# Kernel tuning notes

Measured on AMD Instinct MI355X. Metric: run time of the kernel, lower is better.

Reference implementation:

```python
import jax, jax.numpy as jnp
import numpy as np

B, T, D = 64, 4096, 256


def setup_inputs() -> dict:
    key = jax.random.key(0)
    k0, k1, k2, k3 = jax.random.split(key, 4)
    q = jax.random.normal(k0, (B, D), dtype=jnp.float32)
    k = jax.random.normal(k1, (B, T, D), dtype=jnp.float32)
    m = jax.random.uniform(k2, (B, T), dtype=jnp.float32)
    # learned params: torch.rand init for weights, zeros for bias
    W = jax.random.uniform(k3, (D, D), dtype=jnp.float32)
    bias = jnp.zeros((1,), dtype=jnp.float32)
    return {"q": q, "k": k, "m": m, "W": W, "bias": bias}


def reference(q, k, m, W, bias):
    # mids = W @ q   (original repeats W over batch; a single einsum suffices)
    mids = jnp.einsum('de,be->bd', W, q)            # [B, D]
    # scores_bt = tanh(k_bt . mids_b + bias)
    scores = jnp.tanh(jnp.einsum('btd,bd->bt', k, mids) + bias)  # [B, T]
    # masked, max-stabilized softmax over time
    scores = scores - jnp.max(scores, axis=1, keepdims=True)
    e = jnp.exp(scores) * m
    attn = e / jnp.sum(e, axis=1, keepdims=True)
    return attn
```

## Files before the change

kernel.cpp:

```cpp
#include <hip/hip_runtime.h>
#include <math.h>


#define BB 64
#define TT 4096
#define DD 256
#define TBLKS 32
#define RPB (TT / TBLKS)
#define GB 8
#define CHUNK (TT / GB)

__device__ __forceinline__ float fast_tanh(float x) {
    float e = __expf(2.0f * x);
    return 1.0f - 2.0f * __builtin_amdgcn_rcpf(1.0f + e);
}

__global__ __launch_bounds__(256) void mids_kernel(const float* __restrict__ q,
                                                   const float* __restrict__ W,
                                                   float* __restrict__ mids) {
    const int b    = blockIdx.x;
    const int seg  = blockIdx.y;
    const int lane = threadIdx.x & 63;
    const int wave = threadIdx.x >> 6;
    const int grp  = lane >> 4;
    const int l16  = lane & 15;

    const float* qb = q + (size_t)b * DD + l16 * 4;
    const float4 qf0 = *(const float4*)(qb + 0);
    const float4 qf1 = *(const float4*)(qb + 64);
    const float4 qf2 = *(const float4*)(qb + 128);
    const float4 qf3 = *(const float4*)(qb + 192);

    const int d0 = seg * 64 + wave * 16;
    #pragma unroll
    for (int g = 0; g < 4; ++g) {
        const int d = d0 + g * 4 + grp;
        const float* wr = W + (size_t)d * DD + l16 * 4;
        const float4 w0 = *(const float4*)(wr + 0);
        const float4 w1 = *(const float4*)(wr + 64);
        const float4 w2 = *(const float4*)(wr + 128);
        const float4 w3 = *(const float4*)(wr + 192);
        float p = w0.x*qf0.x + w0.y*qf0.y + w0.z*qf0.z + w0.w*qf0.w;
        p += w1.x*qf1.x + w1.y*qf1.y + w1.z*qf1.z + w1.w*qf1.w;
        p += w2.x*qf2.x + w2.y*qf2.y + w2.z*qf2.z + w2.w*qf2.w;
        p += w3.x*qf3.x + w3.y*qf3.y + w3.z*qf3.z + w3.w*qf3.w;
        p += __shfl_xor(p, 1, 64);
        p += __shfl_xor(p, 2, 64);
        p += __shfl_xor(p, 4, 64);
        p += __shfl_xor(p, 8, 64);
        if (l16 == 0) mids[b * DD + d] = p;
    }
}

__global__ __launch_bounds__(256) void scores_kernel(const float* __restrict__ k,
                                                     const float* __restrict__ mids,
                                                     const float* __restrict__ bias,
                                                     float* __restrict__ scores,
                                                     float* __restrict__ partmax) {
    const int b    = blockIdx.x;
    const int tb   = blockIdx.y;
    const int lane = threadIdx.x & 63;
    const int wave = threadIdx.x >> 6;
    const int grp  = lane >> 4;
    const int l16  = lane & 15;
    const float bv = bias[0];

    const float* mb = mids + (size_t)b * DD + l16 * 4;
    const float4 mf0 = *(const float4*)(mb + 0);
    const float4 mf1 = *(const float4*)(mb + 64);
    const float4 mf2 = *(const float4*)(mb + 128);
    const float4 mf3 = *(const float4*)(mb + 192);

    const int t0 = tb * RPB + wave * 32;
    const float* kbase = k + ((size_t)b * TT + t0) * DD + l16 * 4;

    float lmax = -2.0f;
    #pragma unroll 2
    for (int g = 0; g < 8; ++g) {
        const int trow = g * 4 + grp;
        const float* kr = kbase + (size_t)trow * DD;
        const float4 k0 = *(const float4*)(kr + 0);
        const float4 k1 = *(const float4*)(kr + 64);
        const float4 k2 = *(const float4*)(kr + 128);
        const float4 k3 = *(const float4*)(kr + 192);
        float p = k0.x*mf0.x + k0.y*mf0.y + k0.z*mf0.z + k0.w*mf0.w;
        p += k1.x*mf1.x + k1.y*mf1.y + k1.z*mf1.z + k1.w*mf1.w;
        p += k2.x*mf2.x + k2.y*mf2.y + k2.z*mf2.z + k2.w*mf2.w;
        p += k3.x*mf3.x + k3.y*mf3.y + k3.z*mf3.z + k3.w*mf3.w;
        p += __shfl_xor(p, 1, 64);
        p += __shfl_xor(p, 2, 64);
        p += __shfl_xor(p, 4, 64);
        p += __shfl_xor(p, 8, 64);
        const float s = fast_tanh(p + bv);
        lmax = fmaxf(lmax, s);
        if (l16 == 0) scores[b * TT + t0 + trow] = s;
    }
    lmax = fmaxf(lmax, __shfl_xor(lmax, 16, 64));
    lmax = fmaxf(lmax, __shfl_xor(lmax, 32, 64));
    __shared__ float wmax[4];
    if (lane == 0) wmax[wave] = lmax;
    __syncthreads();
    if (threadIdx.x == 0)
        partmax[b * TBLKS + tb] =
            fmaxf(fmaxf(wmax[0], wmax[1]), fmaxf(wmax[2], wmax[3]));
}

__global__ __launch_bounds__(256) void exp_kernel(const float* __restrict__ scores,
                                                  const float* __restrict__ m,
                                                  const float* __restrict__ partmax,
                                                  float* __restrict__ out,
                                                  float* __restrict__ blocksum) {
    const int b    = blockIdx.x;
    const int g    = blockIdx.y;
    const int tid  = threadIdx.x;
    const int lane = tid & 63;
    const int wave = tid >> 6;
    __shared__ float smax;
    __shared__ float wsum[4];

    if (wave == 0) {
        float mv = (lane < TBLKS) ? partmax[b * TBLKS + lane] : -2.0f;
        #pragma unroll
        for (int off = 16; off; off >>= 1) mv = fmaxf(mv, __shfl_xor(mv, off, 64));
        if (lane == 0) smax = mv;
    }
    __syncthreads();
    const float maxv = smax;

    const int idx = b * TT + g * CHUNK + tid * 2;
    const float2 sv = *(const float2*)(scores + idx);
    const float2 mv2 = *(const float2*)(m + idx);
    const float e0 = __expf(sv.x - maxv) * mv2.x;
    const float e1 = __expf(sv.y - maxv) * mv2.y;
    *(float2*)(out + idx) = make_float2(e0, e1);

    float local = e0 + e1;
    #pragma unroll
    for (int off = 32; off; off >>= 1) local += __shfl_xor(local, off, 64);
    if (lane == 0) wsum[wave] = local;
    __syncthreads();
    if (tid == 0)
        blocksum[b * GB + g] = wsum[0] + wsum[1] + wsum[2] + wsum[3];
}

__global__ __launch_bounds__(256) void norm_kernel(const float* __restrict__ blocksum,
                                                   float* __restrict__ out) {
    const int b   = blockIdx.x;
    const int g   = blockIdx.y;
    const int tid = threadIdx.x;
    float s = 0.0f;
    #pragma unroll
    for (int i = 0; i < GB; ++i) s += blocksum[b * GB + i];
    const float inv = 1.0f / s;
    const int idx = b * TT + g * CHUNK + tid * 2;
    float2 v = *(const float2*)(out + idx);
    v.x *= inv; v.y *= inv;
    *(float2*)(out + idx) = v;
}

extern "C" void kernel_launch(void* const* d_in, const int* in_sizes, int n_in,
                              void* d_out, int out_size, void* d_ws, size_t ws_size,
                              hipStream_t stream) {
    const float* q    = (const float*)d_in[0];
    const float* k    = (const float*)d_in[1];
    const float* m    = (const float*)d_in[2];
    const float* W    = (const float*)d_in[3];
    const float* bias = (const float*)d_in[4];
    float* out = (float*)d_out;

    float* ws       = (float*)d_ws;
    float* mids     = ws;
    float* scores   = mids + BB * DD;
    float* partmax  = scores + BB * TT;
    float* blocksum = partmax + BB * TBLKS;

    mids_kernel<<<dim3(BB, 4), 256, 0, stream>>>(q, W, mids);
    scores_kernel<<<dim3(BB, TBLKS), 256, 0, stream>>>(k, mids, bias, scores, partmax);
    exp_kernel<<<dim3(BB, GB), 256, 0, stream>>>(scores, m, partmax, out, blocksum);
    norm_kernel<<<dim3(BB, GB), 256, 0, stream>>>(blocksum, out);
}
```

Before: 398.1 us.

## Fuse scores and exp kernels, drop max pass, prefetch k rows, DPP reductions

Merges the score and exp kernels into one pass that computes exp(tanh(.))·mask directly and writes partial sums. The max-subtraction step is dropped because tanh is bounded, which removes a kernel launch and the round trip of the scores buffer. Adds register double-buffering of k rows and swaps the shuffle reductions for DPP row reductions. mids_kernel is also split across more blocks. Skipping the max is numerically safe because the scores lie in [-1,1].

```diff
diff --git a/kernel.cpp b/kernel.cpp
--- a/kernel.cpp
+++ b/kernel.cpp
@@ -9,6 +9,20 @@
 #define RPB (TT / TBLKS)
 #define GB 8
 #define CHUNK (TT / GB)
+
+template<int CTRL>
+__device__ __forceinline__ float dpp_add(float x) {
+    int xi = __builtin_bit_cast(int, x);
+    int yi = __builtin_amdgcn_update_dpp(0, xi, CTRL, 0xF, 0xF, true);
+    return x + __builtin_bit_cast(float, yi);
+}
+__device__ __forceinline__ float row16_sum(float p) {
+    p = dpp_add<0xB1>(p);
+    p = dpp_add<0x4E>(p);
+    p = dpp_add<0x141>(p);
+    p = dpp_add<0x140>(p);
+    return p;
+}
 
 __device__ __forceinline__ float fast_tanh(float x) {
     float e = __expf(2.0f * x);
@@ -31,32 +45,26 @@
     const float4 qf2 = *(const float4*)(qb + 128);
     const float4 qf3 = *(const float4*)(qb + 192);
 
-    const int d0 = seg * 64 + wave * 16;
-    #pragma unroll
-    for (int g = 0; g < 4; ++g) {
-        const int d = d0 + g * 4 + grp;
-        const float* wr = W + (size_t)d * DD + l16 * 4;
-        const float4 w0 = *(const float4*)(wr + 0);
-        const float4 w1 = *(const float4*)(wr + 64);
-        const float4 w2 = *(const float4*)(wr + 128);
-        const float4 w3 = *(const float4*)(wr + 192);
-        float p = w0.x*qf0.x + w0.y*qf0.y + w0.z*qf0.z + w0.w*qf0.w;
-        p += w1.x*qf1.x + w1.y*qf1.y + w1.z*qf1.z + w1.w*qf1.w;
-        p += w2.x*qf2.x + w2.y*qf2.y + w2.z*qf2.z + w2.w*qf2.w;
-        p += w3.x*qf3.x + w3.y*qf3.y + w3.z*qf3.z + w3.w*qf3.w;
-        p += __shfl_xor(p, 1, 64);
-        p += __shfl_xor(p, 2, 64);
-        p += __shfl_xor(p, 4, 64);
-        p += __shfl_xor(p, 8, 64);
-        if (l16 == 0) mids[b * DD + d] = p;
-    }
+    const int d = seg * 16 + wave * 4 + grp;
+    const float* wr = W + (size_t)d * DD + l16 * 4;
+    const float4 w0 = *(const float4*)(wr + 0);
+    const float4 w1 = *(const float4*)(wr + 64);
+    const float4 w2 = *(const float4*)(wr + 128);
+    const float4 w3 = *(const float4*)(wr + 192);
+    float p = w0.x*qf0.x + w0.y*qf0.y + w0.z*qf0.z + w0.w*qf0.w;
+    p += w1.x*qf1.x + w1.y*qf1.y + w1.z*qf1.z + w1.w*qf1.w;
+    p += w2.x*qf2.x + w2.y*qf2.y + w2.z*qf2.z + w2.w*qf2.w;
+    p += w3.x*qf3.x + w3.y*qf3.y + w3.z*qf3.z + w3.w*qf3.w;
+    p = row16_sum(p);
+    if (l16 == 0) mids[b * DD + d] = p;
 }
 
-__global__ __launch_bounds__(256) void scores_kernel(const float* __restrict__ k,
-                                                     const float* __restrict__ mids,
-                                                     const float* __restrict__ bias,
-                                                     float* __restrict__ scores,
-                                                     float* __restrict__ partmax) {
+__global__ __launch_bounds__(256) void fused_kernel(const float* __restrict__ k,
+                                                    const float* __restrict__ mids,
+                                                    const float* __restrict__ m,
+                                                    const float* __restrict__ bias,
+                                                    float* __restrict__ out,
+                                                    float* __restrict__ blocksum) {
     const int b    = blockIdx.x;
     const int tb   = blockIdx.y;
     const int lane = threadIdx.x & 63;
@@ -73,74 +81,48 @@
 
     const int t0 = tb * RPB + wave * 32;
     const float* kbase = k + ((size_t)b * TT + t0) * DD + l16 * 4;
+    const float* mrow  = m + (size_t)b * TT + t0;
+    float* orow        = out + (size_t)b * TT + t0;
 
-    float lmax = -2.0f;
-    #pragma unroll 2
+    float4 c0, c1, c2, c3, n0, n1, n2, n3;
+    {
+        const float* kr = kbase + (size_t)grp * DD;
+        c0 = *(const float4*)(kr + 0);
+        c1 = *(const float4*)(kr + 64);
+        c2 = *(const float4*)(kr + 128);
+        c3 = *(const float4*)(kr + 192);
+    }
+    float esum = 0.0f;
+    #pragma unroll
     for (int g = 0; g < 8; ++g) {
-        const int trow = g * 4 + grp;
-        const float* kr = kbase + (size_t)trow * DD;
-        const float4 k0 = *(const float4*)(kr + 0);
-        const float4 k1 = *(const float4*)(kr + 64);
-        const float4 k2 = *(const float4*)(kr + 128);
-        const float4 k3 = *(const float4*)(kr + 192);
-        float p = k0.x*mf0.x + k0.y*mf0.y + k0.z*mf0.z + k0.w*mf0.w;
-        p += k1.x*mf1.x + k1.y*mf1.y + k1.z*mf1.z + k1.w*mf1.w;
-        p += k2.x*mf2.x + k2.y*mf2.y + k2.z*mf2.z + k2.w*mf2.w;
-        p += k3.x*mf3.x + k3.y*mf3.y + k3.z*mf3.z + k3.w*mf3.w;
-        p += __shfl_xor(p, 1, 64);
-        p += __shfl_xor(p, 2, 64);
-        p += __shfl_xor(p, 4, 64);
-        p += __shfl_xor(p, 8, 64);
+        if (g < 7) {
+            const float* kr = kbase + (size_t)((g + 1) * 4 + grp) * DD;
+            n0 = *(const float4*)(kr + 0);
+            n1 = *(const float4*)(kr + 64);
+            n2 = *(const float4*)(kr + 128);
+            n3 = *(const float4*)(kr + 192);
+        }
+        float p = c0.x*mf0.x + c0.y*mf0.y + c0.z*mf0.z + c0.w*mf0.w;
+        p += c1.x*mf1.x + c1.y*mf1.y + c1.z*mf1.z + c1.w*mf1.w;
+        p += c2.x*mf2.x + c2.y*mf2.y + c2.z*mf2.z + c2.w*mf2.w;
+        p += c3.x*mf3.x + c3.y*mf3.y + c3.z*mf3.z + c3.w*mf3.w;
+        p = row16_sum(p);
         const float s = fast_tanh(p + bv);
-        lmax = fmaxf(lmax, s);
-        if (l16 == 0) scores[b * TT + t0 + trow] = s;
+        if (l16 == 0) {
+            const int trow = g * 4 + grp;
+            const float e = __expf(s) * mrow[trow];
+            orow[trow] = e;
+            esum += e;
+        }
+        c0 = n0; c1 = n1; c2 = n2; c3 = n3;
     }
-    lmax = fmaxf(lmax, __shfl_xor(lmax, 16, 64));
-    lmax = fmaxf(lmax, __shfl_xor(lmax, 32, 64));
-    __shared__ float wmax[4];
-    if (lane == 0) wmax[wave] = lmax;
+    esum += __shfl_xor(esum, 16, 64);
+    esum += __shfl_xor(esum, 32, 64);
+    __shared__ float wsum[4];
+    if (lane == 0) wsum[wave] = esum;
     __syncthreads();
     if (threadIdx.x == 0)
-        partmax[b * TBLKS + tb] =
-            fmaxf(fmaxf(wmax[0], wmax[1]), fmaxf(wmax[2], wmax[3]));
-}
-
-__global__ __launch_bounds__(256) void exp_kernel(const float* __restrict__ scores,
-                                                  const float* __restrict__ m,
-                                                  const float* __restrict__ partmax,
-                                                  float* __restrict__ out,
-                                                  float* __restrict__ blocksum) {
-    const int b    = blockIdx.x;
-    const int g    = blockIdx.y;
-    const int tid  = threadIdx.x;
-    const int lane = tid & 63;
-    const int wave = tid >> 6;
-    __shared__ float smax;
-    __shared__ float wsum[4];
-
-    if (wave == 0) {
-        float mv = (lane < TBLKS) ? partmax[b * TBLKS + lane] : -2.0f;
-        #pragma unroll
-        for (int off = 16; off; off >>= 1) mv = fmaxf(mv, __shfl_xor(mv, off, 64));
-        if (lane == 0) smax = mv;
-    }
-    __syncthreads();
-    const float maxv = smax;
-
-    const int idx = b * TT + g * CHUNK + tid * 2;
-    const float2 sv = *(const float2*)(scores + idx);
-    const float2 mv2 = *(const float2*)(m + idx);
-    const float e0 = __expf(sv.x - maxv) * mv2.x;
-    const float e1 = __expf(sv.y - maxv) * mv2.y;
-    *(float2*)(out + idx) = make_float2(e0, e1);
-
-    float local = e0 + e1;
-    #pragma unroll
-    for (int off = 32; off; off >>= 1) local += __shfl_xor(local, off, 64);
-    if (lane == 0) wsum[wave] = local;
-    __syncthreads();
-    if (tid == 0)
-        blocksum[b * GB + g] = wsum[0] + wsum[1] + wsum[2] + wsum[3];
+        blocksum[b * TBLKS + tb] = (wsum[0] + wsum[1]) + (wsum[2] + wsum[3]);
 }
 
 __global__ __launch_bounds__(256) void norm_kernel(const float* __restrict__ blocksum,
@@ -150,7 +132,7 @@
     const int tid = threadIdx.x;
     float s = 0.0f;
     #pragma unroll
-    for (int i = 0; i < GB; ++i) s += blocksum[b * GB + i];
+    for (int i = 0; i < TBLKS; ++i) s += blocksum[b * TBLKS + i];
     const float inv = 1.0f / s;
     const int idx = b * TT + g * CHUNK + tid * 2;
     float2 v = *(const float2*)(out + idx);
@@ -170,12 +152,9 @@
 
     float* ws       = (float*)d_ws;
     float* mids     = ws;
-    float* scores   = mids + BB * DD;
-    float* partmax  = scores + BB * TT;
-    float* blocksum = partmax + BB * TBLKS;
+    float* blocksum = mids + BB * DD;
 
-    mids_kernel<<<dim3(BB, 4), 256, 0, stream>>>(q, W, mids);
-    scores_kernel<<<dim3(BB, TBLKS), 256, 0, stream>>>(k, mids, bias, scores, partmax);
-    exp_kernel<<<dim3(BB, GB), 256, 0, stream>>>(scores, m, partmax, out, blocksum);
+    mids_kernel<<<dim3(BB, 16), 256, 0, stream>>>(q, W, mids);
+    fused_kernel<<<dim3(BB, TBLKS), 256, 0, stream>>>(k, mids, m, bias, out, blocksum);
     norm_kernel<<<dim3(BB, GB), 256, 0, stream>>>(blocksum, out);
 }
```

Measured after the change: 395.5 us. No clear change (-0.7%).
